# Optimization experiments

Measured on AMD Instinct MI355X. Metric: run time of the kernel, lower is better.

Reference implementation:

```python
import jax, jax.numpy as jnp
import numpy as np

N_NODES = 50000


def sage_conv(x, src, dst, W_l, W_r, b):
    # mean-aggregate neighbor features: out_i = W_l @ mean_{j->i} x_j + W_r @ x_i + b
    msg_sum = jax.ops.segment_sum(x[src], dst, num_segments=N_NODES)   # [N, F]
    cnt = jax.ops.segment_sum(jnp.ones_like(dst, dtype=x.dtype), dst, num_segments=N_NODES)
    mean = msg_sum / jnp.maximum(cnt, 1.0)[:, None]                    # zero for isolated nodes
    return mean @ W_l + x @ W_r + b


def setup_inputs() -> dict:
    key = jax.random.key(0)
    ks = jax.random.split(key, 8)
    in_dim, hid, out_dim = 128, 128, 128
    x = jax.random.normal(ks[0], (N_NODES, in_dim), dtype=jnp.float32)
    edge_index = jax.random.randint(ks[1], (2, 800000), 0, N_NODES, dtype=jnp.int64)
    s0 = 1.0 / np.sqrt(in_dim)
    s1 = 1.0 / np.sqrt(hid)
    return {
        "x": x,
        "edge_index": edge_index,
        "W_l0": jax.random.uniform(ks[2], (in_dim, hid), jnp.float32, -s0, s0),
        "W_r0": jax.random.uniform(ks[3], (in_dim, hid), jnp.float32, -s0, s0),
        "b0": jnp.zeros((hid,), jnp.float32),
        "W_l1": jax.random.uniform(ks[4], (hid, out_dim), jnp.float32, -s1, s1),
        "W_r1": jax.random.uniform(ks[5], (hid, out_dim), jnp.float32, -s1, s1),
        "b1": jnp.zeros((out_dim,), jnp.float32),
    }


def reference(x, edge_index, W_l0, W_r0, b0, W_l1, W_r1, b1):
    src, dst = edge_index[0], edge_index[1]
    h = sage_conv(x, src, dst, W_l0, W_r0, b0)
    h = jax.nn.relu(h)
    out = sage_conv(h, src, dst, W_l1, W_r1, b1)
    return out
```

## Files before the change

### kernel.cpp

```cpp
#include <hip/hip_runtime.h>

#define FDIM 128
#define NGRP 8

typedef __attribute__((ext_vector_type(4))) float f32x4;
typedef __attribute__((ext_vector_type(8))) short s16x8;
typedef __attribute__((ext_vector_type(4))) short s16x4;

__device__ inline unsigned short f2bf(float f) {
    unsigned u = __builtin_bit_cast(unsigned, f);
    u += 0x7FFFu + ((u >> 16) & 1u);
    return (unsigned short)(u >> 16);
}
__device__ inline float bflo(unsigned u) { return __builtin_bit_cast(float, u << 16); }
__device__ inline float bfhi(unsigned u) { return __builtin_bit_cast(float, u & 0xFFFF0000u); }


__global__ void hist8_kernel(const int* __restrict__ dst, int* __restrict__ degg, int E, int N) {
    int e = blockIdx.x * blockDim.x + threadIdx.x;
    if (e < E) atomicAdd(&degg[(blockIdx.x & 7) * N + dst[e]], 1);
}

__global__ void scanA1_kernel(const int* __restrict__ in, int* __restrict__ out,
                              int* __restrict__ bsum, int M) {
    __shared__ int s[256];
    int base = blockIdx.x * 1024 + threadIdx.x * 4;
    int4 v = make_int4(0, 0, 0, 0);
    if (base + 3 < M) v = *reinterpret_cast<const int4*>(in + base);
    else {
        if (base + 0 < M) v.x = in[base + 0];
        if (base + 1 < M) v.y = in[base + 1];
        if (base + 2 < M) v.z = in[base + 2];
        if (base + 3 < M) v.w = in[base + 3];
    }
    int tsum = v.x + v.y + v.z + v.w;
    s[threadIdx.x] = tsum;
    __syncthreads();
    for (int off = 1; off < 256; off <<= 1) {
        int t = (threadIdx.x >= off) ? s[threadIdx.x - off] : 0;
        __syncthreads();
        s[threadIdx.x] += t;
        __syncthreads();
    }
    int excl = s[threadIdx.x] - tsum;
    int4 o;
    o.x = excl; o.y = excl + v.x; o.z = o.y + v.y; o.w = o.z + v.z;
    if (base + 3 < M) *reinterpret_cast<int4*>(out + base) = o;
    else {
        if (base + 0 < M) out[base + 0] = o.x;
        if (base + 1 < M) out[base + 1] = o.y;
        if (base + 2 < M) out[base + 2] = o.z;
    }
    if (threadIdx.x == 255) bsum[blockIdx.x] = s[255];
}

__global__ void scanA2_kernel(int* __restrict__ bsum, int nb) {
    __shared__ int s[512];
    int v = (threadIdx.x < (unsigned)nb) ? bsum[threadIdx.x] : 0;
    s[threadIdx.x] = v;
    __syncthreads();
    for (int off = 1; off < 512; off <<= 1) {
        int t = (threadIdx.x >= off) ? s[threadIdx.x - off] : 0;
        __syncthreads();
        s[threadIdx.x] += t;
        __syncthreads();
    }
    if (threadIdx.x < (unsigned)nb) bsum[threadIdx.x] = s[threadIdx.x] - v;
}

__global__ void scanA3_kernel(int* __restrict__ off, int* __restrict__ cursor,
                              const int* __restrict__ bsum, int M, int E) {
    int base = blockIdx.x * 1024 + threadIdx.x * 4;
    int b = bsum[blockIdx.x];
    if (base + 3 < M) {
        int4 v = *reinterpret_cast<const int4*>(off + base);
        v.x += b; v.y += b; v.z += b; v.w += b;
        *reinterpret_cast<int4*>(off + base) = v;
        *reinterpret_cast<int4*>(cursor + base) = v;
    } else {
#pragma unroll
        for (int j = 0; j < 4; ++j)
            if (base + j < M) { int t = off[base + j] + b; off[base + j] = t; cursor[base + j] = t; }
    }
    if (base == 0) off[M] = E;
}

__global__ void rp_kernel(const int* __restrict__ off, int* __restrict__ rp, int N, int E) {
    __shared__ int S0;
    if (threadIdx.x == 0) {
        int s = 0;
#pragma unroll
        for (int g = 0; g < NGRP; ++g) s += off[g * N];
        S0 = s;
    }
    __syncthreads();
    int i = blockIdx.x * 256 + threadIdx.x;
    if (i < N) {
        int s = 0;
#pragma unroll
        for (int g = 0; g < NGRP; ++g) s += off[g * N + i];
        rp[i] = s - S0;
    } else if (i == N) {
        rp[N] = E;
    }
}

__global__ void fill8_kernel(const int* __restrict__ src, const int* __restrict__ dst,
                             int* __restrict__ cursor, int* __restrict__ eidt, int E, int N) {
    int e = blockIdx.x * blockDim.x + threadIdx.x;
    if (e < E) {
        int p = atomicAdd(&cursor[(blockIdx.x & 7) * N + dst[e]], 1);
        eidt[p] = src[e];
    }
}

__global__ void merge_kernel(const int* __restrict__ off, const int* __restrict__ eidt,
                             const int* __restrict__ rp, int* __restrict__ eid, int N) {
    int i = blockIdx.x * 256 + threadIdx.x;
    if (i >= N) return;
    int dp = rp[i];
#pragma unroll
    for (int g = 0; g < NGRP; ++g) {
        int b = off[g * N + i];
        int e2 = off[g * N + i + 1];
        for (int k = b; k < e2; ++k) eid[dp++] = eidt[k];
    }
}

__global__ void prep_x_kernel(const float* __restrict__ x, short* __restrict__ xb, int n4) {
    int i = blockIdx.x * blockDim.x + threadIdx.x;
    if (i < n4) {
        float4 v = reinterpret_cast<const float4*>(x)[i];
        s16x4 o;
        o[0] = (short)f2bf(v.x); o[1] = (short)f2bf(v.y);
        o[2] = (short)f2bf(v.z); o[3] = (short)f2bf(v.w);
        reinterpret_cast<s16x4*>(xb)[i] = o;
    }
}

__global__ void prep_w_kernel(const float* __restrict__ Wl0, const float* __restrict__ Wr0,
                              const float* __restrict__ Wl1, const float* __restrict__ Wr1,
                              short* __restrict__ Wt0, short* __restrict__ Wt1) {
    int g = blockIdx.x * blockDim.x + threadIdx.x;
    int n = g & 127;
    int k = (g >> 7) & 255;
    int layer = g >> 15;
    const float* Wl = layer ? Wl1 : Wl0;
    const float* Wr = layer ? Wr1 : Wr0;
    short* Wt = layer ? Wt1 : Wt0;
    float v = (k < 128) ? Wl[k * 128 + n] : Wr[(k - 128) * 128 + n];
    Wt[n * 256 + k] = (short)f2bf(v);
}

#define ACC8(v) { a[0]+=bflo(v.x); a[1]+=bfhi(v.x); a[2]+=bflo(v.y); a[3]+=bfhi(v.y); \
                  a[4]+=bflo(v.z); a[5]+=bfhi(v.z); a[6]+=bflo(v.w); a[7]+=bfhi(v.w); }

__global__ void gather_kernel(const short* __restrict__ X, const int* __restrict__ rp,
                              const int* __restrict__ eid, short* __restrict__ mb, int N) {
    int node = blockIdx.x * (blockDim.x >> 6) + (threadIdx.x >> 6);
    int lane = threadIdx.x & 63;
    int g = lane >> 4;
    int c = lane & 15;
    if (node >= N) return;
    int beg = rp[node], end = rp[node + 1];
    float a[8];
#pragma unroll
    for (int j = 0; j < 8; ++j) a[j] = 0.0f;

    int k = beg;
    for (; k + 8 <= end; k += 8) {
        int s0 = eid[k + g];
        int s1 = eid[k + 4 + g];
        uint4 v0 = *reinterpret_cast<const uint4*>(X + (size_t)s0 * FDIM + c * 8);
        uint4 v1 = *reinterpret_cast<const uint4*>(X + (size_t)s1 * FDIM + c * 8);
        ACC8(v0);
        ACC8(v1);
    }
    if (k + 4 <= end) {
        int s0 = eid[k + g];
        uint4 v0 = *reinterpret_cast<const uint4*>(X + (size_t)s0 * FDIM + c * 8);
        ACC8(v0);
        k += 4;
    }
    int rem = end - k;
    if (g < rem) {
        int s0 = eid[k + g];
        uint4 v0 = *reinterpret_cast<const uint4*>(X + (size_t)s0 * FDIM + c * 8);
        ACC8(v0);
    }

#pragma unroll
    for (int j = 0; j < 8; ++j) a[j] += __shfl_xor(a[j], 16);
#pragma unroll
    for (int j = 0; j < 8; ++j) a[j] += __shfl_xor(a[j], 32);

    if (g == 0) {
        float inv = (end > beg) ? 1.0f / (float)(end - beg) : 0.0f;
        uint4 o;
        o.x = (unsigned)f2bf(a[0] * inv) | ((unsigned)f2bf(a[1] * inv) << 16);
        o.y = (unsigned)f2bf(a[2] * inv) | ((unsigned)f2bf(a[3] * inv) << 16);
        o.z = (unsigned)f2bf(a[4] * inv) | ((unsigned)f2bf(a[5] * inv) << 16);
        o.w = (unsigned)f2bf(a[6] * inv) | ((unsigned)f2bf(a[7] * inv) << 16);
        *reinterpret_cast<uint4*>(mb + (size_t)node * FDIM + c * 8) = o;
    }
}

template <bool RELU, bool OUTF32>
__global__ __launch_bounds__(256, 2)
void gemm_mfma_kernel(const short* __restrict__ Am, const short* Ax,
                      const short* __restrict__ Wt, const float* __restrict__ bias,
                      float* outf, short* outb, int n) {
    __shared__ short A_lds[64 * 256];
    const int tid = threadIdx.x;
    const int w = tid >> 6, l = tid & 63;
    const int row0 = blockIdx.x * 64;

    s16x8 bfr[8][2];
    {
        const short* wb = Wt + ((32 * w + (l & 15)) * 256 + 8 * (l >> 4));
#pragma unroll
        for (int kc = 0; kc < 8; ++kc)
#pragma unroll
            for (int cf = 0; cf < 2; ++cf)
                bfr[kc][cf] = *reinterpret_cast<const s16x8*>(wb + cf * 16 * 256 + kc * 32);
    }

#pragma unroll
    for (int i = 0; i < 8; ++i) {
        int c = tid + 256 * i;
        int r = c >> 5;
        int ck = c & 31;
        int row = row0 + r;
        s16x8 v;
        if (row < n) {
            const short* sp = (ck < 16) ? (Am + (size_t)row * FDIM + ck * 8)
                                        : (Ax + (size_t)row * FDIM + (ck - 16) * 8);
            v = *reinterpret_cast<const s16x8*>(sp);
        } else {
#pragma unroll
            for (int j = 0; j < 8; ++j) v[j] = 0;
        }
        int byte = r * 512 + ((ck * 16) ^ ((r & 7) << 4));
        *reinterpret_cast<s16x8*>(reinterpret_cast<char*>(A_lds) + byte) = v;
    }
    __syncthreads();

    f32x4 acc[4][2];
    {
        float b0 = bias[32 * w + (l & 15)];
        float b1 = bias[32 * w + 16 + (l & 15)];
#pragma unroll
        for (int rf = 0; rf < 4; ++rf)
#pragma unroll
            for (int i = 0; i < 4; ++i) { acc[rf][0][i] = b0; acc[rf][1][i] = b1; }
    }

    const int arow = l & 15;
    const int aq16 = 16 * (l >> 4);
#pragma unroll
    for (int kc = 0; kc < 8; ++kc) {
        s16x8 afr[4];
#pragma unroll
        for (int rf = 0; rf < 4; ++rf) {
            int r = 16 * rf + arow;
            int kbyte = 64 * kc + aq16;
            int byte = r * 512 + (kbyte ^ ((r & 7) << 4));
            afr[rf] = *reinterpret_cast<const s16x8*>(reinterpret_cast<const char*>(A_lds) + byte);
        }
#pragma unroll
        for (int rf = 0; rf < 4; ++rf)
#pragma unroll
            for (int cf = 0; cf < 2; ++cf)
                acc[rf][cf] = __builtin_amdgcn_mfma_f32_16x16x32_bf16(afr[rf], bfr[kc][cf], acc[rf][cf], 0, 0, 0);
    }

    const int ocol = 32 * w + (l & 15);
    const int orow = 4 * (l >> 4);
#pragma unroll
    for (int rf = 0; rf < 4; ++rf)
#pragma unroll
        for (int cf = 0; cf < 2; ++cf)
#pragma unroll
            for (int i = 0; i < 4; ++i) {
                int row = row0 + 16 * rf + orow + i;
                if (row < n) {
                    float v = acc[rf][cf][i];
                    if (RELU) v = fmaxf(v, 0.0f);
                    if (OUTF32) outf[(size_t)row * FDIM + ocol + 16 * cf] = v;
                    else        outb[(size_t)row * FDIM + ocol + 16 * cf] = (short)f2bf(v);
                }
            }
}

__global__ void degree_kernel(const int* __restrict__ dst, float* __restrict__ cnt, int E) {
    int e = blockIdx.x * blockDim.x + threadIdx.x;
    if (e < E) atomicAdd(&cnt[dst[e]], 1.0f);
}

__global__ void scatter_kernel(const float* __restrict__ x, const int* __restrict__ src,
                               const int* __restrict__ dst, float* __restrict__ msg, int E) {
    int gt = blockIdx.x * blockDim.x + threadIdx.x;
    int e = gt >> 6;
    int lane = gt & 63;
    if (e >= E) return;
    int s = src[e];
    int d = dst[e];
    float2 v = reinterpret_cast<const float2*>(x + (size_t)s * FDIM)[lane];
    float* md = msg + (size_t)d * FDIM + 2 * lane;
    atomicAdd(md, v.x);
    atomicAdd(md + 1, v.y);
}

template <bool RELU>
__global__ void gemm_kernel(const float* agg, const float* cnt,
                            const float* __restrict__ xin, const float* __restrict__ Wl,
                            const float* __restrict__ Wr, const float* __restrict__ bias,
                            float* out, int n) {
    const int ROWS = 16;
    __shared__ float m_s[ROWS][FDIM];
    __shared__ float x_s[ROWS][FDIM];
    int tid = threadIdx.x;
    int row0 = blockIdx.x * ROWS;
#pragma unroll
    for (int i = 0; i < 2; ++i) {
        int idx4 = tid + i * 256;
        int r = idx4 >> 5;
        int c4 = idx4 & 31;
        int row = row0 + r;
        if (row < n) {
            float inv = cnt ? 1.0f / fmaxf(cnt[row], 1.0f) : 1.0f;
            float4 mv = reinterpret_cast<const float4*>(agg + (size_t)row * FDIM)[c4];
            float4 xv = reinterpret_cast<const float4*>(xin + (size_t)row * FDIM)[c4];
            float* mp = &m_s[r][c4 * 4];
            mp[0] = mv.x * inv; mp[1] = mv.y * inv; mp[2] = mv.z * inv; mp[3] = mv.w * inv;
            float* xp = &x_s[r][c4 * 4];
            xp[0] = xv.x; xp[1] = xv.y; xp[2] = xv.z; xp[3] = xv.w;
        }
    }
    __syncthreads();
    int j = tid & 127;
    int rh = tid >> 7;
    float acc[8];
    float bj = bias[j];
#pragma unroll
    for (int r = 0; r < 8; ++r) acc[r] = bj;
#pragma unroll 4
    for (int k = 0; k < FDIM; ++k) {
        float wl = Wl[k * FDIM + j];
        float wr = Wr[k * FDIM + j];
#pragma unroll
        for (int r = 0; r < 8; ++r)
            acc[r] += m_s[rh * 8 + r][k] * wl + x_s[rh * 8 + r][k] * wr;
    }
#pragma unroll
    for (int r = 0; r < 8; ++r) {
        int row = row0 + rh * 8 + r;
        if (row < n) {
            float v = acc[r];
            if (RELU) v = fmaxf(v, 0.0f);
            out[(size_t)row * FDIM + j] = v;
        }
    }
}

extern "C" void kernel_launch(void* const* d_in, const int* in_sizes, int n_in,
                              void* d_out, int out_size, void* d_ws, size_t ws_size,
                              hipStream_t stream) {
    const float* x   = (const float*)d_in[0];
    const int*   ei  = (const int*)d_in[1];
    const float* Wl0 = (const float*)d_in[2];
    const float* Wr0 = (const float*)d_in[3];
    const float* b0  = (const float*)d_in[4];
    const float* Wl1 = (const float*)d_in[5];
    const float* Wr1 = (const float*)d_in[6];
    const float* b1  = (const float*)d_in[7];

    int N = in_sizes[0] / FDIM;
    int E = in_sizes[1] / 2;
    const int* src = ei;
    const int* dst = ei + E;

    size_t featBytes  = (size_t)N * FDIM * sizeof(float);
    size_t featBytesB = (size_t)N * FDIM * sizeof(short);
    int edgeBlocks = (E + 255) / 256;
    int M = NGRP * N;
    int blocksA = (M + 1023) / 1024;

    const size_t o_bsum = 0x0;
    const size_t o_rp   = 0x1000;
    const size_t o_wt0  = 0x33000;
    const size_t o_wt1  = 0x43000;
    const size_t o_eid  = 0x53000;
    const size_t o_xb   = 0x361000;
    const size_t o_mb   = o_xb + featBytesB;
    const size_t need   = o_mb + featBytesB;
    const size_t s_degg = o_mb + 0x0;
    const size_t s_off  = o_mb + 0x187000;
    const size_t s_cur  = o_mb + 0x30E000;
    const size_t s_eidt = o_mb + 0x495000;

    if (ws_size >= need) {
        int*   bsum   = (int*)((char*)d_ws + o_bsum);
        int*   rp     = (int*)((char*)d_ws + o_rp);
        short* Wt0    = (short*)((char*)d_ws + o_wt0);
        short* Wt1    = (short*)((char*)d_ws + o_wt1);
        int*   eid    = (int*)((char*)d_ws + o_eid);
        short* xb     = (short*)((char*)d_ws + o_xb);
        short* mb     = (short*)((char*)d_ws + o_mb);
        int*   degg   = (int*)((char*)d_ws + s_degg);
        int*   off    = (int*)((char*)d_ws + s_off);
        int*   cursor = (int*)((char*)d_ws + s_cur);
        int*   eidt   = (int*)((char*)d_ws + s_eidt);
        float* outF   = (float*)d_out;

        hipMemsetAsync(degg, 0, (size_t)M * sizeof(int), stream);
        hist8_kernel<<<edgeBlocks, 256, 0, stream>>>(dst, degg, E, N);
        scanA1_kernel<<<blocksA, 256, 0, stream>>>(degg, off, bsum, M);
        scanA2_kernel<<<1, 512, 0, stream>>>(bsum, blocksA);
        scanA3_kernel<<<blocksA, 256, 0, stream>>>(off, cursor, bsum, M, E);
        rp_kernel<<<(N + 256) / 256, 256, 0, stream>>>(off, rp, N, E);
        fill8_kernel<<<edgeBlocks, 256, 0, stream>>>(src, dst, cursor, eidt, E, N);
        merge_kernel<<<(N + 255) / 256, 256, 0, stream>>>(off, eidt, rp, eid, N);

        prep_w_kernel<<<256, 256, 0, stream>>>(Wl0, Wr0, Wl1, Wr1, Wt0, Wt1);
        prep_x_kernel<<<(N * FDIM / 4 + 255) / 256, 256, 0, stream>>>(x, xb, N * FDIM / 4);

        int gatherBlocks = (N + 3) / 4;
        int gemmBlocks   = (N + 63) / 64;
        gather_kernel<<<gatherBlocks, 256, 0, stream>>>(xb, rp, eid, mb, N);
        gemm_mfma_kernel<true, false><<<gemmBlocks, 256, 0, stream>>>(mb, xb, Wt0, b0, nullptr, xb, N);
        gather_kernel<<<gatherBlocks, 256, 0, stream>>>(xb, rp, eid, mb, N);
        gemm_mfma_kernel<false, true><<<gemmBlocks, 256, 0, stream>>>(mb, xb, Wt1, b1, outF, nullptr, N);
    } else {
        float* cnt = (float*)d_ws;
        float* h   = (float*)((char*)d_ws + (1 << 18));
        float* msg = (float*)d_out;
        int gemmBlocks = (N + 15) / 16;

        hipMemsetAsync(cnt, 0, (size_t)N * sizeof(float), stream);
        degree_kernel<<<edgeBlocks, 256, 0, stream>>>(dst, cnt, E);

        hipMemsetAsync(msg, 0, featBytes, stream);
        scatter_kernel<<<(E * 64 + 255) / 256, 256, 0, stream>>>(x, src, dst, msg, E);
        gemm_kernel<true><<<gemmBlocks, 256, 0, stream>>>(msg, cnt, x, Wl0, Wr0, b0, h, N);

        hipMemsetAsync(msg, 0, featBytes, stream);
        scatter_kernel<<<(E * 64 + 255) / 256, 256, 0, stream>>>(h, src, dst, msg, E);
        gemm_kernel<false><<<gemmBlocks, 256, 0, stream>>>(msg, cnt, h, Wl1, Wr1, b1, msg, N);
    }
}
```

Baseline: 199.3 us.

## Fuse prologue kernels, merge scan passes, unroll gather, raise GEMM occupancy

```diff
diff --git a/kernel.cpp b/kernel.cpp
--- a/kernel.cpp
+++ b/kernel.cpp
@@ -15,6 +15,37 @@
 __device__ inline float bflo(unsigned u) { return __builtin_bit_cast(float, u << 16); }
 __device__ inline float bfhi(unsigned u) { return __builtin_bit_cast(float, u & 0xFFFF0000u); }
 
+__global__ void prologue_kernel(int4* __restrict__ degg4, int nz,
+                                const float* __restrict__ x, short* __restrict__ xb, int n4x,
+                                const float* __restrict__ Wl0, const float* __restrict__ Wr0,
+                                const float* __restrict__ Wl1, const float* __restrict__ Wr1,
+                                short* __restrict__ Wt0, short* __restrict__ Wt1,
+                                int ZB, int XB) {
+    int bid = blockIdx.x;
+    if (bid < ZB) {
+        int i = bid * 256 + threadIdx.x;
+        if (i < nz) degg4[i] = make_int4(0, 0, 0, 0);
+    } else if (bid < ZB + XB) {
+        int i = (bid - ZB) * 256 + threadIdx.x;
+        if (i < n4x) {
+            float4 v = reinterpret_cast<const float4*>(x)[i];
+            s16x4 o;
+            o[0] = (short)f2bf(v.x); o[1] = (short)f2bf(v.y);
+            o[2] = (short)f2bf(v.z); o[3] = (short)f2bf(v.w);
+            reinterpret_cast<s16x4*>(xb)[i] = o;
+        }
+    } else {
+        int g = (bid - ZB - XB) * 256 + threadIdx.x;
+        int n = g & 127;
+        int k = (g >> 7) & 255;
+        int layer = g >> 15;
+        const float* Wl = layer ? Wl1 : Wl0;
+        const float* Wr = layer ? Wr1 : Wr0;
+        short* Wt = layer ? Wt1 : Wt0;
+        float v = (k < 128) ? Wl[k * 128 + n] : Wr[(k - 128) * 128 + n];
+        Wt[n * 256 + k] = (short)f2bf(v);
+    }
+}
 
 __global__ void hist8_kernel(const int* __restrict__ dst, int* __restrict__ degg, int E, int N) {
     int e = blockIdx.x * blockDim.x + threadIdx.x;
@@ -54,33 +85,31 @@
     if (threadIdx.x == 255) bsum[blockIdx.x] = s[255];
 }
 
-__global__ void scanA2_kernel(int* __restrict__ bsum, int nb) {
-    __shared__ int s[512];
-    int v = (threadIdx.x < (unsigned)nb) ? bsum[threadIdx.x] : 0;
-    s[threadIdx.x] = v;
+__global__ void scanA3_kernel(int* __restrict__ off, int* __restrict__ cursor,
+                              const int* __restrict__ bsum, int nb, int M, int E) {
+    __shared__ int s[256];
+    int t = threadIdx.x;
+    int v = 0;
+    if (t < blockIdx.x) v += bsum[t];
+    if (t + 256 < blockIdx.x) v += bsum[t + 256];
+    s[t] = v;
     __syncthreads();
-    for (int off = 1; off < 512; off <<= 1) {
-        int t = (threadIdx.x >= off) ? s[threadIdx.x - off] : 0;
+    for (int off2 = 128; off2 > 0; off2 >>= 1) {
+        if (t < off2) s[t] += s[t + off2];
         __syncthreads();
-        s[threadIdx.x] += t;
-        __syncthreads();
-    }
-    if (threadIdx.x < (unsigned)nb) bsum[threadIdx.x] = s[threadIdx.x] - v;
-}
-
-__global__ void scanA3_kernel(int* __restrict__ off, int* __restrict__ cursor,
-                              const int* __restrict__ bsum, int M, int E) {
-    int base = blockIdx.x * 1024 + threadIdx.x * 4;
-    int b = bsum[blockIdx.x];
+    }
+    int b = s[0];
+
+    int base = blockIdx.x * 1024 + t * 4;
     if (base + 3 < M) {
-        int4 v = *reinterpret_cast<const int4*>(off + base);
-        v.x += b; v.y += b; v.z += b; v.w += b;
-        *reinterpret_cast<int4*>(off + base) = v;
-        *reinterpret_cast<int4*>(cursor + base) = v;
+        int4 w = *reinterpret_cast<const int4*>(off + base);
+        w.x += b; w.y += b; w.z += b; w.w += b;
+        *reinterpret_cast<int4*>(off + base) = w;
+        *reinterpret_cast<int4*>(cursor + base) = w;
     } else {
 #pragma unroll
         for (int j = 0; j < 4; ++j)
-            if (base + j < M) { int t = off[base + j] + b; off[base + j] = t; cursor[base + j] = t; }
+            if (base + j < M) { int q = off[base + j] + b; off[base + j] = q; cursor[base + j] = q; }
     }
     if (base == 0) off[M] = E;
 }
@@ -125,31 +154,6 @@
         int e2 = off[g * N + i + 1];
         for (int k = b; k < e2; ++k) eid[dp++] = eidt[k];
     }
-}
-
-__global__ void prep_x_kernel(const float* __restrict__ x, short* __restrict__ xb, int n4) {
-    int i = blockIdx.x * blockDim.x + threadIdx.x;
-    if (i < n4) {
-        float4 v = reinterpret_cast<const float4*>(x)[i];
-        s16x4 o;
-        o[0] = (short)f2bf(v.x); o[1] = (short)f2bf(v.y);
-        o[2] = (short)f2bf(v.z); o[3] = (short)f2bf(v.w);
-        reinterpret_cast<s16x4*>(xb)[i] = o;
-    }
-}
-
-__global__ void prep_w_kernel(const float* __restrict__ Wl0, const float* __restrict__ Wr0,
-                              const float* __restrict__ Wl1, const float* __restrict__ Wr1,
-                              short* __restrict__ Wt0, short* __restrict__ Wt1) {
-    int g = blockIdx.x * blockDim.x + threadIdx.x;
-    int n = g & 127;
-    int k = (g >> 7) & 255;
-    int layer = g >> 15;
-    const float* Wl = layer ? Wl1 : Wl0;
-    const float* Wr = layer ? Wr1 : Wr0;
-    short* Wt = layer ? Wt1 : Wt0;
-    float v = (k < 128) ? Wl[k * 128 + n] : Wr[(k - 128) * 128 + n];
-    Wt[n * 256 + k] = (short)f2bf(v);
 }
 
 #define ACC8(v) { a[0]+=bflo(v.x); a[1]+=bfhi(v.x); a[2]+=bflo(v.y); a[3]+=bfhi(v.y); \
@@ -168,13 +172,24 @@
     for (int j = 0; j < 8; ++j) a[j] = 0.0f;
 
     int k = beg;
-    for (; k + 8 <= end; k += 8) {
+    for (; k + 16 <= end; k += 16) {
+        int s0 = eid[k + g];
+        int s1 = eid[k + 4 + g];
+        int s2 = eid[k + 8 + g];
+        int s3 = eid[k + 12 + g];
+        uint4 v0 = *reinterpret_cast<const uint4*>(X + (size_t)s0 * FDIM + c * 8);
+        uint4 v1 = *reinterpret_cast<const uint4*>(X + (size_t)s1 * FDIM + c * 8);
+        uint4 v2 = *reinterpret_cast<const uint4*>(X + (size_t)s2 * FDIM + c * 8);
+        uint4 v3 = *reinterpret_cast<const uint4*>(X + (size_t)s3 * FDIM + c * 8);
+        ACC8(v0); ACC8(v1); ACC8(v2); ACC8(v3);
+    }
+    if (k + 8 <= end) {
         int s0 = eid[k + g];
         int s1 = eid[k + 4 + g];
         uint4 v0 = *reinterpret_cast<const uint4*>(X + (size_t)s0 * FDIM + c * 8);
         uint4 v1 = *reinterpret_cast<const uint4*>(X + (size_t)s1 * FDIM + c * 8);
-        ACC8(v0);
-        ACC8(v1);
+        ACC8(v0); ACC8(v1);
+        k += 8;
     }
     if (k + 4 <= end) {
         int s0 = eid[k + g];
@@ -206,7 +221,7 @@
 }
 
 template <bool RELU, bool OUTF32>
-__global__ __launch_bounds__(256, 2)
+__global__ __launch_bounds__(256, 3)
 void gemm_mfma_kernel(const short* __restrict__ Am, const short* Ax,
                       const short* __restrict__ Wt, const float* __restrict__ bias,
                       float* outf, short* outb, int n) {
@@ -399,7 +414,7 @@
     const size_t s_cur  = o_mb + 0x30E000;
     const size_t s_eidt = o_mb + 0x495000;
 
-    if (ws_size >= need) {
+    if (ws_size >= need && blocksA <= 512) {
         int*   bsum   = (int*)((char*)d_ws + o_bsum);
         int*   rp     = (int*)((char*)d_ws + o_rp);
         short* Wt0    = (short*)((char*)d_ws + o_wt0);
@@ -413,17 +428,20 @@
         int*   eidt   = (int*)((char*)d_ws + s_eidt);
         float* outF   = (float*)d_out;
 
-        hipMemsetAsync(degg, 0, (size_t)M * sizeof(int), stream);
+        int nz  = M / 4;
+        int n4x = N * FDIM / 4;
+        int ZB = (nz + 255) / 256;
+        int XB = (n4x + 255) / 256;
+        int WB = (65536 + 255) / 256;
+        prologue_kernel<<<ZB + XB + WB, 256, 0, stream>>>(
+            (int4*)degg, nz, x, xb, n4x, Wl0, Wr0, Wl1, Wr1, Wt0, Wt1, ZB, XB);
+
         hist8_kernel<<<edgeBlocks, 256, 0, stream>>>(dst, degg, E, N);
         scanA1_kernel<<<blocksA, 256, 0, stream>>>(degg, off, bsum, M);
-        scanA2_kernel<<<1, 512, 0, stream>>>(bsum, blocksA);
-        scanA3_kernel<<<blocksA, 256, 0, stream>>>(off, cursor, bsum, M, E);
+        scanA3_kernel<<<blocksA, 256, 0, stream>>>(off, cursor, bsum, blocksA, M, E);
         rp_kernel<<<(N + 256) / 256, 256, 0, stream>>>(off, rp, N, E);
         fill8_kernel<<<edgeBlocks, 256, 0, stream>>>(src, dst, cursor, eidt, E, N);
         merge_kernel<<<(N + 255) / 256, 256, 0, stream>>>(off, eidt, rp, eid, N);
-
-        prep_w_kernel<<<256, 256, 0, stream>>>(Wl0, Wr0, Wl1, Wr1, Wt0, Wt1);
-        prep_x_kernel<<<(N * FDIM / 4 + 255) / 256, 256, 0, stream>>>(x, xb, N * FDIM / 4);
 
         int gatherBlocks = (N + 3) / 4;
         int gemmBlocks   = (N + 63) / 64;
```

Result: faster. 188.5 us, median of 2 (-5.4%).
